# Performance work log

Measured on AMD Instinct MI355X. Metric: run time of the kernel, lower is better.

## Reference

```python
import jax, jax.numpy as jnp
import numpy as np

N_TOK = 256
C_Z = 128
C = 32
N_HEAD = 4


def setup_inputs() -> dict:
    key = jax.random.key(0)
    ks = jax.random.split(key, 8)
    s = 0.02
    return {
        "z": jax.random.normal(ks[0], (N_TOK, N_TOK, C_Z), dtype=jnp.float32),
        "single_mask": jnp.ones((N_TOK,), dtype=jnp.float32),
        "ln_gamma": jnp.ones((C_Z,), dtype=jnp.float32),
        "ln_beta": jnp.zeros((C_Z,), dtype=jnp.float32),
        "W_q": jax.random.normal(ks[1], (C_Z, N_HEAD * C), dtype=jnp.float32) * s,
        "W_k": jax.random.normal(ks[2], (C_Z, N_HEAD * C), dtype=jnp.float32) * s,
        "W_v": jax.random.normal(ks[3], (C_Z, N_HEAD * C), dtype=jnp.float32) * s,
        "W_b": jax.random.normal(ks[4], (C_Z, N_HEAD), dtype=jnp.float32) * s,
        "W_g": jax.random.normal(ks[5], (C_Z, N_HEAD * C), dtype=jnp.float32) * s,
        "W_out": jax.random.normal(ks[6], (N_HEAD * C, C_Z), dtype=jnp.float32) * s,
    }


def reference(z, single_mask, ln_gamma, ln_beta, W_q, W_k, W_v, W_b, W_g, W_out):
    # LayerNorm over c_z
    mu = jnp.mean(z, axis=-1, keepdims=True)
    var = jnp.var(z, axis=-1, keepdims=True)
    zn = (z - mu) * jax.lax.rsqrt(var + 1e-5) * ln_gamma + ln_beta

    n = zn.shape[0]
    proj = lambda W: (zn @ W).reshape(n, n, N_HEAD, C)
    q = proj(W_q)
    k = proj(W_k)
    v = proj(W_v)
    g = proj(W_g)
    b = zn @ W_b  # [i, j, h] -> used as bias b[j, k, h]

    # a[i,j,k,h] = q[i,j]·k[i,k]/sqrt(c) + b[j,k,h]
    a = jnp.einsum('ijhc,ikhc->ijkh', q, k) / np.sqrt(C).astype(np.float32)
    a = a + b[None, :, :, :]
    a = a + (-1e9) * (1.0 - single_mask)[None, None, :, None]
    a = jax.nn.softmax(a, axis=-2)  # over k

    o = jnp.einsum('ijkh,ikhc->ijhc', a, v)
    o = jax.nn.sigmoid(g) * o
    o = o.reshape(n, n, N_HEAD * C)
    return o @ W_out
```

## Files before the change

kernel.cpp:

```cpp
#include <hip/hip_runtime.h>
#include <hip/hip_bf16.h>

#define NT 256
#define CZ 128
#define CH 32
#define NH 4
#define PL 2097152

typedef unsigned short ushort_t;
typedef unsigned int uint_t;
typedef __attribute__((ext_vector_type(8))) short short8;
typedef __attribute__((ext_vector_type(4))) float f32x4;

__device__ __forceinline__ float bfbits2f(uint_t bits){
  union { uint_t u; float f; } v; v.u = bits; return v.f;
}
__device__ __forceinline__ float bf2f(ushort_t u){
  return bfbits2f(((uint_t)u) << 16);
}
__device__ __forceinline__ ushort_t f2bf(float f){
  union { float f; uint_t u; } v; v.f = f;
  uint_t u = v.u;
  uint_t r = (u + 0x7fffu + ((u >> 16) & 1u)) >> 16;
  return (ushort_t)r;
}
__device__ __forceinline__ void unpk(uint_t w, float& lo, float& hi){
  lo = bfbits2f(w << 16);
  hi = bfbits2f(w & 0xffff0000u);
}
__device__ __forceinline__ short8 as_s8(uint4 u){
  union { uint4 u; short8 s; } v; v.u = u; return v.s;
}
__device__ __forceinline__ int detect_f32(const ushort_t* zz){
  int l = threadIdx.x & 63;
  int bad = 0;
  #pragma unroll
  for(int s=0;s<4;s++){
    float v = bf2f(zz[l*4 + s]);
    if(!(fabsf(v) < 1e9f)) bad = 1;
  }
  return (__ballot(bad) != 0ull) ? 1 : 0;
}

__global__ void k_cvt_small(const void* __restrict__ m_, const void* __restrict__ g_,
    const void* __restrict__ b_, const void* __restrict__ wb_,
    float* __restrict__ dst, const ushort_t* __restrict__ zz){
  int isf32 = detect_f32(zz);
  int idx = threadIdx.x * 4;
  const void* sp; int off;
  if(idx < 256){ sp = m_;  off = idx; }
  else if(idx < 384){ sp = g_;  off = idx-256; }
  else if(idx < 512){ sp = b_;  off = idx-384; }
  else { sp = wb_; off = idx-512; }
  float4 o;
  if(isf32){ o = *(const float4*)((const float*)sp + off); }
  else {
    uint2 u = *(const uint2*)((const ushort_t*)sp + off);
    unpk(u.x, o.x, o.y); unpk(u.y, o.z, o.w);
  }
  *(float4*)(dst + idx) = o;
}

__global__ __launch_bounds__(256) void k_cvt_wt(const void* __restrict__ s0,
    const void* __restrict__ s1, const void* __restrict__ s2,
    const void* __restrict__ s3, const void* __restrict__ s4,
    ushort_t* __restrict__ dst, const ushort_t* __restrict__ zz){
  int isf32 = detect_f32(zz);
  const void* srcs[5] = {s0,s1,s2,s3,s4};
  int w = blockIdx.x >> 6;
  int idx = (blockIdx.x & 63)*256 + threadIdx.x;
  int k = idx >> 7, c = idx & 127;
  const void* sp = srcs[w];
  float v;
  if(isf32) v = ((const float*)sp)[idx];
  else      v = bf2f(((const ushort_t*)sp)[idx]);
  dst[(size_t)w*16384 + (size_t)c*128 + k] = f2bf(v);
}

__global__ __launch_bounds__(256) void k_lnproj(const void* __restrict__ zraw,
    const float* __restrict__ smallf, const ushort_t* __restrict__ Wt,
    ushort_t* __restrict__ qh, ushort_t* __restrict__ kh,
    ushort_t* __restrict__ vh, ushort_t* __restrict__ gh,
    float* __restrict__ btm){
  __shared__ __align__(16) char lds[47104];
  ushort_t* znl = (ushort_t*)lds;
  float*    tbB = (float*)(lds + 34816);
  float*    wbs = (float*)(lds + 45056);
  const float* mkf = smallf;
  const float* gmf = smallf + 256;
  const float* btf = smallf + 384;
  const float* Wbf = smallf + 512;
  int t = threadIdx.x;
  int isf32 = detect_f32((const ushort_t*)zraw);
  wbs[t] = Wbf[t]; wbs[t+256] = Wbf[t+256];
  __syncthreads();

  int row_loc = t >> 1, half = t & 1;
  size_t r = (size_t)blockIdx.x*128 + row_loc;
  float mval = -1e9f * (1.f - mkf[r & 255]);
  float s = 0.f, s2 = 0.f;
  if(isf32){
    const float4* zp = (const float4*)((const float*)zraw + r*CZ + half*64);
    #pragma unroll
    for(int q=0;q<16;q++){
      float4 v = zp[q];
      s  += (v.x + v.y) + (v.z + v.w);
      s2 += (v.x*v.x + v.y*v.y) + (v.z*v.z + v.w*v.w);
    }
  } else {
    const uint4* zp = (const uint4*)((const ushort_t*)zraw + r*CZ + half*64);
    #pragma unroll
    for(int q=0;q<8;q++){
      uint4 u = zp[q];
      const uint_t* pu = (const uint_t*)&u;
      #pragma unroll
      for(int e=0;e<4;e++){
        float lo, hi; unpk(pu[e], lo, hi);
        s += lo + hi; s2 += lo*lo + hi*hi;
      }
    }
  }
  s  += __shfl_xor(s, 1);
  s2 += __shfl_xor(s2, 1);
  float mu  = s * (1.f/CZ);
  float var = fmaxf(s2 * (1.f/CZ) - mu*mu, 0.f);
  float rs  = rsqrtf(var + 1e-5f);
  float acch[4] = {0.f,0.f,0.f,0.f};
  #pragma unroll
  for(int chunk=0;chunk<8;chunk++){
    float v8[8];
    if(isf32){
      const float4* zp = (const float4*)((const float*)zraw + r*CZ + half*64 + chunk*8);
      float4 a = zp[0], b = zp[1];
      v8[0]=a.x; v8[1]=a.y; v8[2]=a.z; v8[3]=a.w;
      v8[4]=b.x; v8[5]=b.y; v8[6]=b.z; v8[7]=b.w;
    } else {
      uint4 u = *(const uint4*)((const ushort_t*)zraw + r*CZ + half*64 + chunk*8);
      const uint_t* pu = (const uint_t*)&u;
      #pragma unroll
      for(int e=0;e<4;e++) unpk(pu[e], v8[e*2], v8[e*2+1]);
    }
    uint_t ow[4];
    #pragma unroll
    for(int e2=0;e2<4;e2++){
      int cg = half*64 + chunk*8 + e2*2;
      float v0 = (v8[e2*2]   - mu)*rs*gmf[cg]   + btf[cg];
      float v1 = (v8[e2*2+1] - mu)*rs*gmf[cg+1] + btf[cg+1];
      float4 w0 = *(const float4*)&wbs[cg*4];
      float4 w1 = *(const float4*)&wbs[(cg+1)*4];
      acch[0] += v0*w0.x + v1*w1.x;
      acch[1] += v0*w0.y + v1*w1.y;
      acch[2] += v0*w0.z + v1*w1.z;
      acch[3] += v0*w0.w + v1*w1.w;
      ow[e2] = (uint_t)f2bf(v0) | ((uint_t)f2bf(v1) << 16);
    }
    uint4 o; o.x=ow[0]; o.y=ow[1]; o.z=ow[2]; o.w=ow[3];
    *(uint4*)(znl + row_loc*136 + half*64 + chunk*8) = o;
  }
  #pragma unroll
  for(int h=0;h<4;h++){
    float tot = acch[h] + __shfl_xor(acch[h], 1);
    if(half == 0) btm[(size_t)h*65536 + r] = tot + mval;
  }
  __syncthreads();

  int wave = t>>6, l = t&63, n = l&15, quad = l>>4;
  uint4 af[2][4];
  #pragma unroll
  for(int mt=0;mt<2;mt++)
    #pragma unroll
    for(int kb=0;kb<4;kb++)
      af[mt][kb] = *(const uint4*)(znl + (wave*32 + mt*16 + n)*136 + kb*32 + quad*8);
  float* T = tbB + wave*640;
  int rrow = l >> 1, rhalf = l & 1;
  ushort_t* outs[4] = {qh, kh, vh, gh};
  size_t row0 = (size_t)blockIdx.x*128 + wave*32;
  #pragma unroll
  for(int w=0;w<4;w++){
    const ushort_t* W = Wt + (size_t)w*16384;
    ushort_t* D = outs[w];
    float sc = (w==0) ? 0.17677669529663687f : 1.f;
    #pragma unroll
    for(int nt=0;nt<8;nt++){
      uint4 bfr[4];
      #pragma unroll
      for(int kb=0;kb<4;kb++)
        bfr[kb] = *(const uint4*)(W + ((size_t)(nt*16 + n))*128 + kb*32 + quad*8);
      f32x4 a0 = {0.f,0.f,0.f,0.f}, a1 = {0.f,0.f,0.f,0.f};
      #pragma unroll
      for(int kb=0;kb<4;kb++){
        a0 = __builtin_amdgcn_mfma_f32_16x16x32_bf16(as_s8(af[0][kb]), as_s8(bfr[kb]), a0, 0,0,0);
        a1 = __builtin_amdgcn_mfma_f32_16x16x32_bf16(as_s8(af[1][kb]), as_s8(bfr[kb]), a1, 0,0,0);
      }
      #pragma unroll
      for(int rr=0;rr<4;rr++){
        T[(quad*4 + rr)*20 + n]      = a0[rr];
        T[(16 + quad*4 + rr)*20 + n] = a1[rr];
      }
      float4 v0 = *(const float4*)(T + rrow*20 + rhalf*8);
      float4 v1 = *(const float4*)(T + rrow*20 + rhalf*8 + 4);
      uint4 o;
      o.x = (uint_t)f2bf(v0.x*sc) | ((uint_t)f2bf(v0.y*sc) << 16);
      o.y = (uint_t)f2bf(v0.z*sc) | ((uint_t)f2bf(v0.w*sc) << 16);
      o.z = (uint_t)f2bf(v1.x*sc) | ((uint_t)f2bf(v1.y*sc) << 16);
      o.w = (uint_t)f2bf(v1.z*sc) | ((uint_t)f2bf(v1.w*sc) << 16);
      *(uint4*)(D + (size_t)(nt>>1)*PL + (row0 + rrow)*CH + (nt&1)*16 + rhalf*8) = o;
    }
  }
}

__global__ __launch_bounds__(256, 4) void k_attn(
    const ushort_t* __restrict__ qh, const ushort_t* __restrict__ kh,
    const ushort_t* __restrict__ vh, const ushort_t* __restrict__ gh,
    const float* __restrict__ btm, ushort_t* __restrict__ oh){
  __shared__ __align__(16) char lds[53248];
  uint4* VfA = (uint4*)lds;
  uint4* Kf  = (uint4*)(lds + 16384);
  ushort_t* Vn = (ushort_t*)(lds + 32768);
  int t = threadIdx.x;
  int i = blockIdx.x >> 2, h = blockIdx.x & 3;
  int wave = t >> 6, l = t & 63;
  int n = l & 15, quad = l >> 4;
  const ushort_t* qhp = qh + (size_t)h*PL + (size_t)(i*NT)*CH;
  const ushort_t* khp = kh + (size_t)h*PL + (size_t)(i*NT)*CH;
  const ushort_t* vhp = vh + (size_t)h*PL + (size_t)(i*NT)*CH;
  const ushort_t* ghp = gh + (size_t)h*PL + (size_t)(i*NT)*CH;
  ushort_t*       ohp = oh + (size_t)h*PL + (size_t)(i*NT)*CH;
  const float*    bth = btm + (size_t)h*65536;

  {
    const uint4* vp = (const uint4*)(vhp + t*CH);
    uint4 u0=vp[0], u1=vp[1], u2=vp[2], u3=vp[3];
    uint4* dstp = (uint4*)(Vn + t*40);
    dstp[0]=u0; dstp[1]=u1; dstp[2]=u2; dstp[3]=u3;
  }
  {
    #pragma unroll
    for(int m=0;m<4;m++){
      int kt = wave*4 + m;
      Kf[kt*64 + l] = *(const uint4*)(khp + (size_t)(kt*16 + n)*CH + quad*8);
    }
  }
  __syncthreads();
  {
    #pragma unroll
    for(int it=0; it<4; it++){
      int u = wave + it*4, kblk = u >> 1, ct = u & 1;
      uint_t d[4];
      #pragma unroll
      for(int e=0;e<4;e++){
        uint_t lo = Vn[(kblk*32 + quad*8 + e*2    )*40 + ct*16 + n];
        uint_t hi = Vn[(kblk*32 + quad*8 + e*2 + 1)*40 + ct*16 + n];
        d[e] = lo | (hi << 16);
      }
      uint4 o; o.x=d[0]; o.y=d[1]; o.z=d[2]; o.w=d[3];
      VfA[u*64 + l] = o;
    }
  }
  __syncthreads();
  ushort_t* Pw = (ushort_t*)(lds + 32768) + wave*2176;

  for(int s=0;s<4;s++){
    int jt = wave*4 + s;
    uint4 qf = *(const uint4*)(qhp + (size_t)(jt*16 + n)*CH + quad*8);
    f32x4 acc[16];
    #pragma unroll
    for(int kt=0;kt<16;kt++)
      acc[kt] = *(const f32x4*)(bth + (size_t)(jt*16 + n)*256 + kt*16 + quad*4);
    #pragma unroll
    for(int kt=0;kt<16;kt++){
      uint4 kfv = Kf[kt*64 + l];
      acc[kt] = __builtin_amdgcn_mfma_f32_16x16x32_bf16(as_s8(kfv), as_s8(qf), acc[kt], 0,0,0);
    }
    float sum0 = 0.f, sum1 = 0.f;
    uint2 pv[16];
    #pragma unroll
    for(int kt=0;kt<16;kt++){
      float e0 = __expf(acc[kt][0]);
      float e1 = __expf(acc[kt][1]);
      float e2 = __expf(acc[kt][2]);
      float e3 = __expf(acc[kt][3]);
      sum0 += e0 + e1; sum1 += e2 + e3;
      pv[kt].x = (uint_t)f2bf(e0) | ((uint_t)f2bf(e1) << 16);
      pv[kt].y = (uint_t)f2bf(e2) | ((uint_t)f2bf(e3) << 16);
    }
    f32x4 oa0 = {0.f,0.f,0.f,0.f}, oa1 = {0.f,0.f,0.f,0.f};
    #pragma unroll
    for(int H=0; H<2; H++){
      #pragma unroll
      for(int kt2=0;kt2<8;kt2++)
        *(uint2*)(Pw + n*136 + kt2*16 + quad*4) = pv[H*8 + kt2];
      #pragma unroll
      for(int kb2=0;kb2<4;kb2++){
        uint4 pf = *(const uint4*)(Pw + n*136 + kb2*32 + quad*8);
        int kg = H*4 + kb2;
        oa0 = __builtin_amdgcn_mfma_f32_16x16x32_bf16(as_s8(VfA[(kg*2+0)*64 + l]), as_s8(pf), oa0, 0,0,0);
        oa1 = __builtin_amdgcn_mfma_f32_16x16x32_bf16(as_s8(VfA[(kg*2+1)*64 + l]), as_s8(pf), oa1, 0,0,0);
      }
    }
    float ssum = sum0 + sum1;
    ssum += __shfl_xor(ssum, 16);
    ssum += __shfl_xor(ssum, 32);
    float inv = 1.f / ssum;
    size_t rb = (size_t)(jt*16 + n)*CH;
    uint2 g0 = *(const uint2*)(ghp + rb + quad*4);
    uint2 g1 = *(const uint2*)(ghp + rb + 16 + quad*4);
    float ga[4], gc[4];
    unpk(g0.x, ga[0], ga[1]); unpk(g0.y, ga[2], ga[3]);
    unpk(g1.x, gc[0], gc[1]); unpk(g1.y, gc[2], gc[3]);
    float v0[4], v1[4];
    #pragma unroll
    for(int rr=0;rr<4;rr++){
      v0[rr] = oa0[rr] * inv * (1.f/(1.f + __expf(-ga[rr])));
      v1[rr] = oa1[rr] * inv * (1.f/(1.f + __expf(-gc[rr])));
    }
    uint2 s0, s1;
    s0.x = (uint_t)f2bf(v0[0]) | ((uint_t)f2bf(v0[1]) << 16);
    s0.y = (uint_t)f2bf(v0[2]) | ((uint_t)f2bf(v0[3]) << 16);
    s1.x = (uint_t)f2bf(v1[0]) | ((uint_t)f2bf(v1[1]) << 16);
    s1.y = (uint_t)f2bf(v1[2]) | ((uint_t)f2bf(v1[3]) << 16);
    *(uint2*)(ohp + rb + quad*4)      = s0;
    *(uint2*)(ohp + rb + 16 + quad*4) = s1;
  }
}

__global__ __launch_bounds__(256) void k_gemm1(const ushort_t* __restrict__ oh,
    const ushort_t* __restrict__ Wt, void* __restrict__ outp,
    const ushort_t* __restrict__ zz){
  __shared__ __align__(16) float tbB[4*640];
  int isf32 = detect_f32(zz);
  int t = threadIdx.x, wave = t>>6, l = t&63, n = l&15, quad = l>>4;
  size_t row0 = (size_t)blockIdx.x*128 + wave*32;
  float* T = tbB + wave*640;
  int rrow = l >> 1, rhalf = l & 1;
  uint4 af[2][4];
  #pragma unroll
  for(int mt=0;mt<2;mt++)
    #pragma unroll
    for(int kb=0;kb<4;kb++)
      af[mt][kb] = *(const uint4*)(oh + (size_t)kb*PL + (row0 + mt*16 + n)*CH + quad*8);
  #pragma unroll
  for(int nt=0;nt<8;nt++){
    uint4 bfr[4];
    #pragma unroll
    for(int kb=0;kb<4;kb++)
      bfr[kb] = *(const uint4*)(Wt + ((size_t)(nt*16 + n))*128 + kb*32 + quad*8);
    f32x4 a0 = {0.f,0.f,0.f,0.f}, a1 = {0.f,0.f,0.f,0.f};
    #pragma unroll
    for(int kb=0;kb<4;kb++){
      a0 = __builtin_amdgcn_mfma_f32_16x16x32_bf16(as_s8(af[0][kb]), as_s8(bfr[kb]), a0, 0,0,0);
      a1 = __builtin_amdgcn_mfma_f32_16x16x32_bf16(as_s8(af[1][kb]), as_s8(bfr[kb]), a1, 0,0,0);
    }
    #pragma unroll
    for(int rr=0;rr<4;rr++){
      T[(quad*4 + rr)*20 + n]      = a0[rr];
      T[(16 + quad*4 + rr)*20 + n] = a1[rr];
    }
    float4 v0 = *(const float4*)(T + rrow*20 + rhalf*8);
    float4 v1 = *(const float4*)(T + rrow*20 + rhalf*8 + 4);
    if(isf32){
      float* of = (float*)outp + (row0 + rrow)*CZ + nt*16 + rhalf*8;
      *(float4*)of = v0;
      *(float4*)(of + 4) = v1;
    } else {
      uint4 o;
      o.x = (uint_t)f2bf(v0.x) | ((uint_t)f2bf(v0.y) << 16);
      o.y = (uint_t)f2bf(v0.z) | ((uint_t)f2bf(v0.w) << 16);
      o.z = (uint_t)f2bf(v1.x) | ((uint_t)f2bf(v1.y) << 16);
      o.w = (uint_t)f2bf(v1.z) | ((uint_t)f2bf(v1.w) << 16);
      *(uint4*)((ushort_t*)outp + (row0 + rrow)*CZ + nt*16 + rhalf*8) = o;
    }
  }
}

extern "C" void kernel_launch(void* const* d_in, const int* in_sizes, int n_in,
                              void* d_out, int out_size, void* d_ws, size_t ws_size,
                              hipStream_t stream){
  char* wsb = (char*)d_ws;
  const size_t TB = (size_t)16777216;
  ushort_t* qh  = (ushort_t*)(wsb);
  ushort_t* kh  = (ushort_t*)(wsb + TB);
  ushort_t* vh  = (ushort_t*)(wsb + 2*TB);
  ushort_t* gh  = (ushort_t*)(wsb + 3*TB);
  ushort_t* oh  = (ushort_t*)(wsb + 4*TB);
  float*    btm = (float*)   (wsb + 5*TB);
  float*  smallf= (float*)   (wsb + 5*TB + (1u<<20));
  ushort_t* Wt  = (ushort_t*)(wsb + 5*TB + (1u<<20) + 4096);
  const ushort_t* zz = (const ushort_t*)d_in[0];

  k_cvt_small<<<1,   256, 0, stream>>>(d_in[1], d_in[2], d_in[3], d_in[7], smallf, zz);
  k_cvt_wt   <<<320, 256, 0, stream>>>(d_in[4], d_in[5], d_in[6], d_in[8], d_in[9], Wt, zz);
  k_lnproj   <<<512, 256, 0, stream>>>(d_in[0], smallf, Wt, qh, kh, vh, gh, btm);
  k_attn     <<<1024,256, 0, stream>>>(qh, kh, vh, gh, btm, oh);
  k_gemm1    <<<512, 256, 0, stream>>>(oh, Wt + (size_t)4*16384, d_out, zz);
}
```

Baseline: 225.3 us.

## Stream attention over key chunks, load K from global, cache bf16 z in LDS

The attention kernel now processes keys in four chunks of 64, so each chunk's logits are turned into probabilities and fed to the PV MFMA right away. This replaces the 16-tile accumulator array and its 16-entry P buffer, cutting register pressure. K fragments are now read straight from global memory instead of being staged in LDS, which shrinks shared memory from 52 KB to 36 KB and allows higher occupancy, at the cost of re-reading K for every query tile. Separately, the layernorm kernel now stores the raw z row as bf16 in LDS during the statistics pass and reads it back for normalization, avoiding a second global read but rounding fp32 inputs to bf16 before normalization.

Result: slower. 252.9 us (+12.3%).

```diff
diff --git a/kernel.cpp b/kernel.cpp
--- a/kernel.cpp
+++ b/kernel.cpp
@@ -102,22 +102,30 @@
   if(isf32){
     const float4* zp = (const float4*)((const float*)zraw + r*CZ + half*64);
     #pragma unroll
-    for(int q=0;q<16;q++){
-      float4 v = zp[q];
-      s  += (v.x + v.y) + (v.z + v.w);
-      s2 += (v.x*v.x + v.y*v.y) + (v.z*v.z + v.w*v.w);
+    for(int q8=0;q8<8;q8++){
+      float4 a = zp[q8*2], b = zp[q8*2+1];
+      s  += (a.x + a.y) + (a.z + a.w) + (b.x + b.y) + (b.z + b.w);
+      s2 += (a.x*a.x + a.y*a.y) + (a.z*a.z + a.w*a.w)
+          + (b.x*b.x + b.y*b.y) + (b.z*b.z + b.w*b.w);
+      uint4 o;
+      o.x = (uint_t)f2bf(a.x) | ((uint_t)f2bf(a.y) << 16);
+      o.y = (uint_t)f2bf(a.z) | ((uint_t)f2bf(a.w) << 16);
+      o.z = (uint_t)f2bf(b.x) | ((uint_t)f2bf(b.y) << 16);
+      o.w = (uint_t)f2bf(b.z) | ((uint_t)f2bf(b.w) << 16);
+      *(uint4*)(znl + row_loc*136 + half*64 + q8*8) = o;
     }
   } else {
     const uint4* zp = (const uint4*)((const ushort_t*)zraw + r*CZ + half*64);
     #pragma unroll
-    for(int q=0;q<8;q++){
-      uint4 u = zp[q];
+    for(int q8=0;q8<8;q8++){
+      uint4 u = zp[q8];
       const uint_t* pu = (const uint_t*)&u;
       #pragma unroll
       for(int e=0;e<4;e++){
         float lo, hi; unpk(pu[e], lo, hi);
         s += lo + hi; s2 += lo*lo + hi*hi;
       }
+      *(uint4*)(znl + row_loc*136 + half*64 + q8*8) = u;
     }
   }
   s  += __shfl_xor(s, 1);
@@ -128,18 +136,11 @@
   float acch[4] = {0.f,0.f,0.f,0.f};
   #pragma unroll
   for(int chunk=0;chunk<8;chunk++){
+    uint4 u = *(const uint4*)(znl + row_loc*136 + half*64 + chunk*8);
+    const uint_t* pu = (const uint_t*)&u;
     float v8[8];
-    if(isf32){
-      const float4* zp = (const float4*)((const float*)zraw + r*CZ + half*64 + chunk*8);
-      float4 a = zp[0], b = zp[1];
-      v8[0]=a.x; v8[1]=a.y; v8[2]=a.z; v8[3]=a.w;
-      v8[4]=b.x; v8[5]=b.y; v8[6]=b.z; v8[7]=b.w;
-    } else {
-      uint4 u = *(const uint4*)((const ushort_t*)zraw + r*CZ + half*64 + chunk*8);
-      const uint_t* pu = (const uint_t*)&u;
-      #pragma unroll
-      for(int e=0;e<4;e++) unpk(pu[e], v8[e*2], v8[e*2+1]);
-    }
+    #pragma unroll
+    for(int e=0;e<4;e++) unpk(pu[e], v8[e*2], v8[e*2+1]);
     uint_t ow[4];
     #pragma unroll
     for(int e2=0;e2<4;e2++){
@@ -213,10 +214,9 @@
     const ushort_t* __restrict__ qh, const ushort_t* __restrict__ kh,
     const ushort_t* __restrict__ vh, const ushort_t* __restrict__ gh,
     const float* __restrict__ btm, ushort_t* __restrict__ oh){
-  __shared__ __align__(16) char lds[53248];
+  __shared__ __align__(16) char lds[36864];
   uint4* VfA = (uint4*)lds;
-  uint4* Kf  = (uint4*)(lds + 16384);
-  ushort_t* Vn = (ushort_t*)(lds + 32768);
+  ushort_t* Vn = (ushort_t*)(lds + 16384);
   int t = threadIdx.x;
   int i = blockIdx.x >> 2, h = blockIdx.x & 3;
   int wave = t >> 6, l = t & 63;
@@ -234,13 +234,6 @@
     uint4* dstp = (uint4*)(Vn + t*40);
     dstp[0]=u0; dstp[1]=u1; dstp[2]=u2; dstp[3]=u3;
   }
-  {
-    #pragma unroll
-    for(int m=0;m<4;m++){
-      int kt = wave*4 + m;
-      Kf[kt*64 + l] = *(const uint4*)(khp + (size_t)(kt*16 + n)*CH + quad*8);
-    }
-  }
   __syncthreads();
   {
     #pragma unroll
@@ -258,42 +251,42 @@
     }
   }
   __syncthreads();
-  ushort_t* Pw = (ushort_t*)(lds + 32768) + wave*2176;
+  ushort_t* Pw = (ushort_t*)(lds + 16384) + wave*1152;
 
   for(int s=0;s<4;s++){
     int jt = wave*4 + s;
     uint4 qf = *(const uint4*)(qhp + (size_t)(jt*16 + n)*CH + quad*8);
-    f32x4 acc[16];
-    #pragma unroll
-    for(int kt=0;kt<16;kt++)
-      acc[kt] = *(const f32x4*)(bth + (size_t)(jt*16 + n)*256 + kt*16 + quad*4);
-    #pragma unroll
-    for(int kt=0;kt<16;kt++){
-      uint4 kfv = Kf[kt*64 + l];
-      acc[kt] = __builtin_amdgcn_mfma_f32_16x16x32_bf16(as_s8(kfv), as_s8(qf), acc[kt], 0,0,0);
-    }
+    const float* brow = bth + (size_t)(jt*16 + n)*256 + quad*4;
     float sum0 = 0.f, sum1 = 0.f;
-    uint2 pv[16];
-    #pragma unroll
-    for(int kt=0;kt<16;kt++){
-      float e0 = __expf(acc[kt][0]);
-      float e1 = __expf(acc[kt][1]);
-      float e2 = __expf(acc[kt][2]);
-      float e3 = __expf(acc[kt][3]);
-      sum0 += e0 + e1; sum1 += e2 + e3;
-      pv[kt].x = (uint_t)f2bf(e0) | ((uint_t)f2bf(e1) << 16);
-      pv[kt].y = (uint_t)f2bf(e2) | ((uint_t)f2bf(e3) << 16);
-    }
     f32x4 oa0 = {0.f,0.f,0.f,0.f}, oa1 = {0.f,0.f,0.f,0.f};
     #pragma unroll
-    for(int H=0; H<2; H++){
-      #pragma unroll
-      for(int kt2=0;kt2<8;kt2++)
-        *(uint2*)(Pw + n*136 + kt2*16 + quad*4) = pv[H*8 + kt2];
-      #pragma unroll
-      for(int kb2=0;kb2<4;kb2++){
-        uint4 pf = *(const uint4*)(Pw + n*136 + kb2*32 + quad*8);
-        int kg = H*4 + kb2;
+    for(int ch=0; ch<4; ch++){
+      f32x4 acc[4];
+      #pragma unroll
+      for(int m=0;m<4;m++)
+        acc[m] = *(const f32x4*)(brow + (ch*4 + m)*16);
+      #pragma unroll
+      for(int m=0;m<4;m++){
+        int kt = ch*4 + m;
+        uint4 kf = *(const uint4*)(khp + (size_t)(kt*16 + n)*CH + quad*8);
+        acc[m] = __builtin_amdgcn_mfma_f32_16x16x32_bf16(as_s8(kf), as_s8(qf), acc[m], 0,0,0);
+      }
+      #pragma unroll
+      for(int m=0;m<4;m++){
+        float e0 = __expf(acc[m][0]);
+        float e1 = __expf(acc[m][1]);
+        float e2 = __expf(acc[m][2]);
+        float e3 = __expf(acc[m][3]);
+        sum0 += e0 + e1; sum1 += e2 + e3;
+        uint2 wv;
+        wv.x = (uint_t)f2bf(e0) | ((uint_t)f2bf(e1) << 16);
+        wv.y = (uint_t)f2bf(e2) | ((uint_t)f2bf(e3) << 16);
+        *(uint2*)(Pw + n*72 + m*16 + quad*4) = wv;
+      }
+      #pragma unroll
+      for(int kb=0;kb<2;kb++){
+        uint4 pf = *(const uint4*)(Pw + n*72 + kb*32 + quad*8);
+        int kg = ch*2 + kb;
         oa0 = __builtin_amdgcn_mfma_f32_16x16x32_bf16(as_s8(VfA[(kg*2+0)*64 + l]), as_s8(pf), oa0, 0,0,0);
         oa1 = __builtin_amdgcn_mfma_f32_16x16x32_bf16(as_s8(VfA[(kg*2+1)*64 + l]), as_s8(pf), oa1, 0,0,0);
       }
```
